# Kernel optimization log

Hardware: AMD Instinct MI355X
Metric: run time of the kernel (lower is better)

Reference implementation:

```python
import jax, jax.numpy as jnp
import numpy as np

NUM_HEADS = 32
NUM_KV = 8
Q_MULT = NUM_HEADS // NUM_KV  # 4
HEAD_DIM = 128
WINDOW = 1024
SM_SCALE = 1.0 / np.sqrt(HEAD_DIM)


def setup_inputs() -> dict:
    key = jax.random.key(0)
    k1, k2, k3, k4 = jax.random.split(key, 4)
    B, S = 2, 2048
    Q = jax.random.normal(k1, (B, S, NUM_HEADS * HEAD_DIM), dtype=jnp.float32)
    K = jax.random.normal(k2, (B, S, NUM_KV * HEAD_DIM), dtype=jnp.float32)
    V = jax.random.normal(k3, (B, S, NUM_KV * HEAD_DIM), dtype=jnp.float32)
    sinks = jax.random.normal(k4, (NUM_HEADS,), dtype=jnp.float32) * 0.1
    return {"Q": Q, "K": K, "V": V, "sinks": sinks}


def reference(Q, K, V, sinks):
    B, S, _ = Q.shape
    # GQA layout: head = kv * q_mult + m (matches Q[b].view(S, kv, q_mult, d))
    Qh = Q.reshape(B, S, NUM_KV, Q_MULT, HEAD_DIM)
    Kh = K.reshape(B, S, NUM_KV, HEAD_DIM)
    Vh = V.reshape(B, S, NUM_KV, HEAD_DIM)

    # scores: [B, kv, q_mult, S_q, S_k]
    scores = jnp.einsum('bqhmd,bkhd->bhmqk', Qh, Kh) * SM_SCALE

    q_idx = jnp.arange(S)[:, None]
    k_idx = jnp.arange(S)[None, :]
    # causal AND within sliding window: q - WINDOW < k <= q
    allowed = (k_idx <= q_idx) & (k_idx > q_idx - WINDOW)
    scores = jnp.where(allowed[None, None, None, :, :], scores, -jnp.inf)

    # learned sink logit per head, appended as an extra softmax column
    sink = sinks.reshape(NUM_KV, Q_MULT)[None, :, :, None, None]
    sink = jnp.broadcast_to(sink, (B, NUM_KV, Q_MULT, S, 1))
    logits = jnp.concatenate([scores, sink], axis=-1)
    w = jax.nn.softmax(logits, axis=-1)[..., :-1]  # drop sink column

    out = jnp.einsum('bhmqk,bkhd->bqhmd', w, Vh)
    return out.reshape(B, S, NUM_HEADS * HEAD_DIM)
```

## Files before the change

kernel.cpp:

```cpp
#include <hip/hip_runtime.h>
#include <stdint.h>

#define S_LEN 2048
#define HD    128
#define NKV   8
#define NQM   4
#define WIN   1024
#define QB    32
#define KTILE 32
#define KVROW (NKV * HD)
#define QROW  (NQM * NKV * HD)

typedef __attribute__((ext_vector_type(8))) short bf16x8;
typedef __attribute__((ext_vector_type(4))) float f32x4;
typedef __attribute__((ext_vector_type(4))) int   i32x4;

__device__ __forceinline__ uint32_t f2bf(float f) {
  uint32_t x = __builtin_bit_cast(uint32_t, f);
  x += 0x7fffu + ((x >> 16) & 1u);
  return x >> 16;
}

__device__ __forceinline__ void load8bf(const uint16_t* p, uint32_t o[4]) {
  i32x4 v = *reinterpret_cast<const i32x4*>(p);
  o[0] = (uint32_t)v[0]; o[1] = (uint32_t)v[1]; o[2] = (uint32_t)v[2]; o[3] = (uint32_t)v[3];
}
__device__ __forceinline__ void load8bf(const float* p, uint32_t o[4]) {
  float4 a = *reinterpret_cast<const float4*>(p);
  float4 b = *reinterpret_cast<const float4*>(p + 4);
  o[0] = f2bf(a.x) | (f2bf(a.y) << 16);
  o[1] = f2bf(a.z) | (f2bf(a.w) << 16);
  o[2] = f2bf(b.x) | (f2bf(b.y) << 16);
  o[3] = f2bf(b.z) | (f2bf(b.w) << 16);
}

__global__ void cvt_kernel(const float* __restrict__ in, uint16_t* __restrict__ out, int n4) {
  int i = blockIdx.x * blockDim.x + threadIdx.x;
  int stride = gridDim.x * blockDim.x;
  for (int j = i; j < n4; j += stride) {
    float4 v = reinterpret_cast<const float4*>(in)[j];
    ushort4 o;
    o.x = (uint16_t)f2bf(v.x); o.y = (uint16_t)f2bf(v.y);
    o.z = (uint16_t)f2bf(v.z); o.w = (uint16_t)f2bf(v.w);
    reinterpret_cast<ushort4*>(out)[j] = o;
  }
}

#define VSWZ(d) (((((uint32_t)(d) >> 3) ^ (uint32_t)(d)) & 7u) << 3)

template <typename KVT>
__launch_bounds__(256, 2)
__global__ void attn_kernel(const float* __restrict__ Q,
                            const KVT* __restrict__ Ksrc,
                            const KVT* __restrict__ Vsrc,
                            const float* __restrict__ sinks,
                            float* __restrict__ out) {
  __shared__ __align__(16) uint8_t smem[40960];

  const int tid  = threadIdx.x;
  const int lane = tid & 63;
  const int wv   = tid >> 6;
  const int c    = lane & 15;
  const int g    = lane >> 4;
  uint8_t* pls = smem + 32768 + wv * 2048;

  const int bid = blockIdx.x;
  const int kv  = bid & 7;
  const int i2  = bid >> 3;
  const int b   = i2 / 48;
  const int pairIdx = i2 % 48;
  const int head = kv * NQM + wv;
  const float sink_l2 = sinks[head] * 1.4426950408889634f;

  int qtA, qtB, nrep;
  if (pairIdx < 16) { qtA = 31 - pairIdx; qtB = pairIdx; nrep = 2; }
  else              { qtA = pairIdx + 16; qtB = 0;       nrep = 1; }

  const int kr  = tid >> 3;
  const int kcB = (tid & 7) * 32;
  const uint32_t kw0 = (uint32_t)(kr * 256 + ((kcB)      ^ ((kr & 7) << 4)));
  const uint32_t kw1 = (uint32_t)(kr * 256 + ((kcB + 16) ^ ((kr & 7) << 4)));
  const KVT* kg = Ksrc + (size_t)(b * S_LEN) * KVROW + kv * HD + (tid & 7) * 16;
  const size_t kbase = (size_t)(b * S_LEN) * KVROW + kv * HD;
  const int va = tid >> 4;
  const int vd = tid & 15;
  const KVT* vg = Vsrc + (size_t)(b * S_LEN) * KVROW + kv * HD + vd * 8;

  uint32_t vr0[4], vr1[4];

  auto stageK = [&](uint8_t* kbuf, int kt) {
    if constexpr (sizeof(KVT) == 2) {
      #pragma unroll
      for (int ch = 0; ch < 2; ++ch) {
        const int o    = wv * 2048 + ch * 1024 + lane * 16;
        const int row  = o >> 8;
        const int scol = (o & 255) ^ ((row & 7) << 4);
        const uint8_t* gp = (const uint8_t*)(Ksrc + kbase + (size_t)(kt + row) * KVROW) + scol;
        __builtin_amdgcn_global_load_lds(
            (const __attribute__((address_space(1))) void*)gp,
            (__attribute__((address_space(3))) void*)(kbuf + wv * 2048 + ch * 1024),
            16, 0, 0);
      }
    } else {
      const KVT* src = kg + (size_t)(kt + kr) * KVROW;
      uint32_t t0[4], t1[4];
      load8bf(src, t0); load8bf(src + 8, t1);
      i32x4 w0, w1;
      w0[0]=(int)t0[0]; w0[1]=(int)t0[1]; w0[2]=(int)t0[2]; w0[3]=(int)t0[3];
      w1[0]=(int)t1[0]; w1[1]=(int)t1[1]; w1[2]=(int)t1[2]; w1[3]=(int)t1[3];
      *reinterpret_cast<i32x4*>(kbuf + kw0) = w0;
      *reinterpret_cast<i32x4*>(kbuf + kw1) = w1;
    }
  };
  auto loadV = [&](int kt) {
    const KVT* vs = vg + (size_t)(kt + 2 * va) * KVROW;
    load8bf(vs, vr0); load8bf(vs + KVROW, vr1);
  };
  auto writeV = [&](uint8_t* vbuf) {
    #pragma unroll
    for (int ii = 0; ii < 8; ++ii) {
      int d = vd * 8 + ii;
      uint32_t lo = (ii & 1) ? (vr0[ii >> 1] >> 16) : (vr0[ii >> 1] & 0xffffu);
      uint32_t hi = (ii & 1) ? (vr1[ii >> 1] >> 16) : (vr1[ii >> 1] & 0xffffu);
      uint32_t byte = (uint32_t)(d * 64) + (((uint32_t)(va * 4)) ^ VSWZ(d));
      *reinterpret_cast<uint32_t*>(vbuf + byte) = lo | (hi << 16);
    }
  };

  const float SCALE2 = 0.08838834764831845f * 1.4426950408889634f;
  const uint32_t sp = ((uint32_t)(c & 7)) << 3;

  for (int rep = 0; rep < nrep; ++rep) {
    const int q0 = (rep ? qtB : qtA) * QB;

    bf16x8 qf[2][4];
    #pragma unroll
    for (int tq = 0; tq < 2; ++tq) {
      const float* qp = Q + (size_t)(b * S_LEN + q0 + tq * 16 + c) * QROW + head * HD;
      #pragma unroll
      for (int f = 0; f < 4; ++f) {
        int d0 = f * 32 + g * 8;
        float4 a = *reinterpret_cast<const float4*>(qp + d0);
        float4 bb = *reinterpret_cast<const float4*>(qp + d0 + 4);
        i32x4 t;
        t[0] = (int)(f2bf(a.x * SCALE2) | (f2bf(a.y * SCALE2) << 16));
        t[1] = (int)(f2bf(a.z * SCALE2) | (f2bf(a.w * SCALE2) << 16));
        t[2] = (int)(f2bf(bb.x * SCALE2) | (f2bf(bb.y * SCALE2) << 16));
        t[3] = (int)(f2bf(bb.z * SCALE2) | (f2bf(bb.w * SCALE2) << 16));
        qf[tq][f] = __builtin_bit_cast(bf16x8, t);
      }
    }

    float m_[2] = {sink_l2, sink_l2};
    float l_[2] = {1.0f, 1.0f};
    f32x4 acc[2][8];
    #pragma unroll
    for (int tq = 0; tq < 2; ++tq)
      #pragma unroll
      for (int dt = 0; dt < 8; ++dt) acc[tq][dt] = (f32x4)0.0f;

    int kstart = q0 - (WIN - 1);
    if (kstart < 0) kstart = 0;
    kstart &= ~(KTILE - 1);

    uint8_t* kcur = smem;         uint8_t* kalt = smem + 8192;
    uint8_t* vcur = smem + 16384; uint8_t* valt = smem + 24576;

    loadV(kstart);
    stageK(kcur, kstart);
    writeV(vcur);
    __syncthreads();

    for (int kt = kstart; kt <= q0; kt += KTILE) {
      const bool more = (kt + KTILE) <= q0;
      if (more) {
        stageK(kalt, kt + KTILE);
        loadV(kt + KTILE);
      }

      f32x4 st[2][2];
      #pragma unroll
      for (int a_ = 0; a_ < 2; ++a_)
        #pragma unroll
        for (int b_ = 0; b_ < 2; ++b_) st[a_][b_] = (f32x4)0.0f;

      __builtin_amdgcn_s_setprio(1);
      #pragma unroll
      for (int kt_ = 0; kt_ < 2; ++kt_) {
        bf16x8 kf[4];
        #pragma unroll
        for (int f = 0; f < 4; ++f) {
          int row = kt_ * 16 + c;
          uint32_t byte = (uint32_t)(row * 256 + ((f * 64 + g * 16) ^ ((row & 7) << 4)));
          kf[f] = *reinterpret_cast<const bf16x8*>(kcur + byte);
        }
        #pragma unroll
        for (int tq = 0; tq < 2; ++tq)
          #pragma unroll
          for (int f = 0; f < 4; ++f)
            st[kt_][tq] = __builtin_amdgcn_mfma_f32_16x16x32_bf16(kf[f], qf[tq][f], st[kt_][tq], 0, 0, 0);
      }
      __builtin_amdgcn_s_setprio(0);

      const bool need_mask = (kt + KTILE - 1 > q0) || (kt < q0 + QB - WIN);
      if (need_mask) {
        #pragma unroll
        for (int kt_ = 0; kt_ < 2; ++kt_)
          #pragma unroll
          for (int tq = 0; tq < 2; ++tq)
            #pragma unroll
            for (int r = 0; r < 4; ++r) {
              int k_ = kt + kt_ * 16 + g * 4 + r;
              int q_ = q0 + tq * 16 + c;
              bool ok = (k_ <= q_) && (k_ > q_ - WIN);
              if (!ok) st[kt_][tq][r] = -1e38f;
            }
      }

      #pragma unroll
      for (int tq = 0; tq < 2; ++tq) {
        float vmax = fmaxf(fmaxf(fmaxf(st[0][tq][0], st[0][tq][1]), fmaxf(st[0][tq][2], st[0][tq][3])),
                           fmaxf(fmaxf(st[1][tq][0], st[1][tq][1]), fmaxf(st[1][tq][2], st[1][tq][3])));
        vmax = fmaxf(vmax, __shfl_xor(vmax, 16));
        vmax = fmaxf(vmax, __shfl_xor(vmax, 32));
        const float mold = m_[tq];
        if (!__all(vmax <= mold + 11.54f)) {
          float mnew = fmaxf(mold, vmax);
          float scl  = exp2f(mold - mnew);
          m_[tq] = mnew;
          l_[tq] *= scl;
          float sc[4];
          #pragma unroll
          for (int r = 0; r < 4; ++r) sc[r] = __shfl(scl, (lane & 48) | (g * 4 + r));
          #pragma unroll
          for (int dt = 0; dt < 8; ++dt)
            #pragma unroll
            for (int r = 0; r < 4; ++r) acc[tq][dt][r] *= sc[r];
        }
        const float mrun = m_[tq];
        float p[2][4];
        float s = 0.0f;
        #pragma unroll
        for (int kt_ = 0; kt_ < 2; ++kt_)
          #pragma unroll
          for (int r = 0; r < 4; ++r) {
            float e = exp2f(st[kt_][tq][r] - mrun);
            p[kt_][r] = e;
            s += e;
          }
        s += __shfl_xor(s, 16);
        s += __shfl_xor(s, 32);
        l_[tq] += s;
        #pragma unroll
        for (int kt_ = 0; kt_ < 2; ++kt_) {
          uint32_t lo = f2bf(p[kt_][0]) | (f2bf(p[kt_][1]) << 16);
          uint32_t hi = f2bf(p[kt_][2]) | (f2bf(p[kt_][3]) << 16);
          uint32_t byte = (uint32_t)((tq * 16 + c) * 64) + (((uint32_t)(kt_ * 32 + g * 8)) ^ sp);
          uint2 pk; pk.x = lo; pk.y = hi;
          *reinterpret_cast<uint2*>(pls + byte) = pk;
        }
      }

      bf16x8 pa[2];
      #pragma unroll
      for (int tq = 0; tq < 2; ++tq) {
        uint32_t base = (uint32_t)((tq * 16 + c) * 64);
        uint2 plo = *reinterpret_cast<const uint2*>(pls + base + (((uint32_t)(g * 16))     ^ sp));
        uint2 phi = *reinterpret_cast<const uint2*>(pls + base + (((uint32_t)(g * 16 + 8)) ^ sp));
        i32x4 pv; pv[0] = (int)plo.x; pv[1] = (int)plo.y; pv[2] = (int)phi.x; pv[3] = (int)phi.y;
        pa[tq] = __builtin_bit_cast(bf16x8, pv);
      }
      __builtin_amdgcn_s_setprio(1);
      #pragma unroll
      for (int dt = 0; dt < 8; ++dt) {
        int d = dt * 16 + c;
        uint32_t rowb = (uint32_t)(d * 64);
        uint32_t swz  = VSWZ(d);
        uint2 lo = *reinterpret_cast<const uint2*>(vcur + rowb + (((uint32_t)(g * 16))     ^ swz));
        uint2 hi = *reinterpret_cast<const uint2*>(vcur + rowb + (((uint32_t)(g * 16 + 8)) ^ swz));
        i32x4 vv; vv[0] = (int)lo.x; vv[1] = (int)lo.y; vv[2] = (int)hi.x; vv[3] = (int)hi.y;
        bf16x8 vf = __builtin_bit_cast(bf16x8, vv);
        #pragma unroll
        for (int tq = 0; tq < 2; ++tq)
          acc[tq][dt] = __builtin_amdgcn_mfma_f32_16x16x32_bf16(pa[tq], vf, acc[tq][dt], 0, 0, 0);
      }
      __builtin_amdgcn_s_setprio(0);

      if (more) writeV(valt);
      __syncthreads();
      uint8_t* t0 = kcur; kcur = kalt; kalt = t0;
      uint8_t* t1 = vcur; vcur = valt; valt = t1;
    }

    #pragma unroll
    for (int tq = 0; tq < 2; ++tq) {
      float linv = 1.0f / l_[tq];
      float li[4];
      #pragma unroll
      for (int r = 0; r < 4; ++r) li[r] = __shfl(linv, (lane & 48) | (g * 4 + r));
      #pragma unroll
      for (int dt = 0; dt < 8; ++dt)
        #pragma unroll
        for (int r = 0; r < 4; ++r) {
          size_t o = (size_t)(b * S_LEN + q0 + tq * 16 + g * 4 + r) * QROW + head * HD + dt * 16 + c;
          out[o] = acc[tq][dt][r] * li[r];
        }
    }
  }
}

extern "C" void kernel_launch(void* const* d_in, const int* in_sizes, int n_in,
                              void* d_out, int out_size, void* d_ws, size_t ws_size,
                              hipStream_t stream) {
  const float* Q     = (const float*)d_in[0];
  const float* K     = (const float*)d_in[1];
  const float* V     = (const float*)d_in[2];
  const float* sinks = (const float*)d_in[3];
  float* out = (float*)d_out;

  const int nK = in_sizes[1];
  const int B  = in_sizes[0] / (S_LEN * QROW);
  dim3 grid(384 * B);

  const size_t need = (size_t)nK * 2u * 2u;
  if (ws_size >= need) {
    uint16_t* Kb = (uint16_t*)d_ws;
    uint16_t* Vb = Kb + nK;
    cvt_kernel<<<1024, 256, 0, stream>>>(K, Kb, nK / 4);
    cvt_kernel<<<1024, 256, 0, stream>>>(V, Vb, nK / 4);
    attn_kernel<uint16_t><<<grid, 256, 0, stream>>>(Q, Kb, Vb, sinks, out);
  } else {
    attn_kernel<float><<<grid, 256, 0, stream>>>(Q, K, V, sinks, out);
  }
}
```

Before: 247.3 us.

## Use packed bf16 convert, lane-local row sums, lazy max reduction, fused K/V conversion

Replaces the manual round-to-nearest bf16 packing with the hardware v_cvt_pk_bf16_f32 instruction, and uses v_perm_b32 to interleave V halves. The per-tile row-sum shuffles are removed: each lane keeps a partial sum (initialised to a quarter of the sink term) and the sum is reduced across lanes once at the end. The row-max cross-lane shuffles now run only when the lane-local max exceeds the threshold. The two K/V conversion launches are merged into one kernel. All of these are meant to cut VALU and shuffle work in the inner loop plus one launch, with a slight rounding-mode dependence on the hardware convert.

After: 226.4 us. -8.4%, faster.

```diff
diff --git a/kernel.cpp b/kernel.cpp
--- a/kernel.cpp
+++ b/kernel.cpp
@@ -21,6 +21,17 @@
   return x >> 16;
 }
 
+__device__ __forceinline__ uint32_t cvtpk(float lo, float hi) {
+  uint32_t r;
+  asm("v_cvt_pk_bf16_f32 %0, %1, %2" : "=v"(r) : "v"(lo), "v"(hi));
+  return r;
+}
+__device__ __forceinline__ uint32_t perm2(uint32_t a, uint32_t b, uint32_t sel) {
+  uint32_t r;
+  asm("v_perm_b32 %0, %1, %2, %3" : "=v"(r) : "v"(a), "v"(b), "s"(sel));
+  return r;
+}
+
 __device__ __forceinline__ void load8bf(const uint16_t* p, uint32_t o[4]) {
   i32x4 v = *reinterpret_cast<const i32x4*>(p);
   o[0] = (uint32_t)v[0]; o[1] = (uint32_t)v[1]; o[2] = (uint32_t)v[2]; o[3] = (uint32_t)v[3];
@@ -28,21 +39,25 @@
 __device__ __forceinline__ void load8bf(const float* p, uint32_t o[4]) {
   float4 a = *reinterpret_cast<const float4*>(p);
   float4 b = *reinterpret_cast<const float4*>(p + 4);
-  o[0] = f2bf(a.x) | (f2bf(a.y) << 16);
-  o[1] = f2bf(a.z) | (f2bf(a.w) << 16);
-  o[2] = f2bf(b.x) | (f2bf(b.y) << 16);
-  o[3] = f2bf(b.z) | (f2bf(b.w) << 16);
-}
-
-__global__ void cvt_kernel(const float* __restrict__ in, uint16_t* __restrict__ out, int n4) {
+  o[0] = cvtpk(a.x, a.y);
+  o[1] = cvtpk(a.z, a.w);
+  o[2] = cvtpk(b.x, b.y);
+  o[3] = cvtpk(b.z, b.w);
+}
+
+__global__ void cvt2_kernel(const float* __restrict__ inK, const float* __restrict__ inV,
+                            uint16_t* __restrict__ outK, uint16_t* __restrict__ outV, int n4) {
   int i = blockIdx.x * blockDim.x + threadIdx.x;
   int stride = gridDim.x * blockDim.x;
-  for (int j = i; j < n4; j += stride) {
-    float4 v = reinterpret_cast<const float4*>(in)[j];
-    ushort4 o;
-    o.x = (uint16_t)f2bf(v.x); o.y = (uint16_t)f2bf(v.y);
-    o.z = (uint16_t)f2bf(v.z); o.w = (uint16_t)f2bf(v.w);
-    reinterpret_cast<ushort4*>(out)[j] = o;
+  for (int j = i; j < 2 * n4; j += stride) {
+    const float* in = (j < n4) ? inK : inV;
+    uint16_t* out   = (j < n4) ? outK : outV;
+    int jj = (j < n4) ? j : j - n4;
+    float4 v = reinterpret_cast<const float4*>(in)[jj];
+    uint2 o;
+    o.x = cvtpk(v.x, v.y);
+    o.y = cvtpk(v.z, v.w);
+    reinterpret_cast<uint2*>(out)[jj] = o;
   }
 }
 
@@ -120,10 +135,10 @@
     #pragma unroll
     for (int ii = 0; ii < 8; ++ii) {
       int d = vd * 8 + ii;
-      uint32_t lo = (ii & 1) ? (vr0[ii >> 1] >> 16) : (vr0[ii >> 1] & 0xffffu);
-      uint32_t hi = (ii & 1) ? (vr1[ii >> 1] >> 16) : (vr1[ii >> 1] & 0xffffu);
+      uint32_t w = (ii & 1) ? perm2(vr1[ii >> 1], vr0[ii >> 1], 0x07060302u)
+                            : perm2(vr1[ii >> 1], vr0[ii >> 1], 0x05040100u);
       uint32_t byte = (uint32_t)(d * 64) + (((uint32_t)(va * 4)) ^ VSWZ(d));
-      *reinterpret_cast<uint32_t*>(vbuf + byte) = lo | (hi << 16);
+      *reinterpret_cast<uint32_t*>(vbuf + byte) = w;
     }
   };
 
@@ -143,16 +158,16 @@
         float4 a = *reinterpret_cast<const float4*>(qp + d0);
         float4 bb = *reinterpret_cast<const float4*>(qp + d0 + 4);
         i32x4 t;
-        t[0] = (int)(f2bf(a.x * SCALE2) | (f2bf(a.y * SCALE2) << 16));
-        t[1] = (int)(f2bf(a.z * SCALE2) | (f2bf(a.w * SCALE2) << 16));
-        t[2] = (int)(f2bf(bb.x * SCALE2) | (f2bf(bb.y * SCALE2) << 16));
-        t[3] = (int)(f2bf(bb.z * SCALE2) | (f2bf(bb.w * SCALE2) << 16));
+        t[0] = (int)cvtpk(a.x * SCALE2, a.y * SCALE2);
+        t[1] = (int)cvtpk(a.z * SCALE2, a.w * SCALE2);
+        t[2] = (int)cvtpk(bb.x * SCALE2, bb.y * SCALE2);
+        t[3] = (int)cvtpk(bb.z * SCALE2, bb.w * SCALE2);
         qf[tq][f] = __builtin_bit_cast(bf16x8, t);
       }
     }
 
     float m_[2] = {sink_l2, sink_l2};
-    float l_[2] = {1.0f, 1.0f};
+    float lp_[2] = {0.25f, 0.25f};
     f32x4 acc[2][8];
     #pragma unroll
     for (int tq = 0; tq < 2; ++tq)
@@ -219,16 +234,16 @@
 
       #pragma unroll
       for (int tq = 0; tq < 2; ++tq) {
-        float vmax = fmaxf(fmaxf(fmaxf(st[0][tq][0], st[0][tq][1]), fmaxf(st[0][tq][2], st[0][tq][3])),
-                           fmaxf(fmaxf(st[1][tq][0], st[1][tq][1]), fmaxf(st[1][tq][2], st[1][tq][3])));
-        vmax = fmaxf(vmax, __shfl_xor(vmax, 16));
-        vmax = fmaxf(vmax, __shfl_xor(vmax, 32));
+        float ownmax = fmaxf(fmaxf(fmaxf(st[0][tq][0], st[0][tq][1]), fmaxf(st[0][tq][2], st[0][tq][3])),
+                             fmaxf(fmaxf(st[1][tq][0], st[1][tq][1]), fmaxf(st[1][tq][2], st[1][tq][3])));
         const float mold = m_[tq];
-        if (!__all(vmax <= mold + 11.54f)) {
+        if (!__all(ownmax <= mold + 11.54f)) {
+          float vmax = fmaxf(ownmax, __shfl_xor(ownmax, 16));
+          vmax = fmaxf(vmax, __shfl_xor(vmax, 32));
           float mnew = fmaxf(mold, vmax);
           float scl  = exp2f(mold - mnew);
           m_[tq] = mnew;
-          l_[tq] *= scl;
+          lp_[tq] *= scl;
           float sc[4];
           #pragma unroll
           for (int r = 0; r < 4; ++r) sc[r] = __shfl(scl, (lane & 48) | (g * 4 + r));
@@ -248,15 +263,13 @@
             p[kt_][r] = e;
             s += e;
           }
-        s += __shfl_xor(s, 16);
-        s += __shfl_xor(s, 32);
-        l_[tq] += s;
+        lp_[tq] += s;
         #pragma unroll
         for (int kt_ = 0; kt_ < 2; ++kt_) {
-          uint32_t lo = f2bf(p[kt_][0]) | (f2bf(p[kt_][1]) << 16);
-          uint32_t hi = f2bf(p[kt_][2]) | (f2bf(p[kt_][3]) << 16);
+          uint2 pk;
+          pk.x = cvtpk(p[kt_][0], p[kt_][1]);
+          pk.y = cvtpk(p[kt_][2], p[kt_][3]);
           uint32_t byte = (uint32_t)((tq * 16 + c) * 64) + (((uint32_t)(kt_ * 32 + g * 8)) ^ sp);
-          uint2 pk; pk.x = lo; pk.y = hi;
           *reinterpret_cast<uint2*>(pls + byte) = pk;
         }
       }
@@ -294,7 +307,10 @@
 
     #pragma unroll
     for (int tq = 0; tq < 2; ++tq) {
-      float linv = 1.0f / l_[tq];
+      float lt = lp_[tq];
+      lt += __shfl_xor(lt, 16);
+      lt += __shfl_xor(lt, 32);
+      float linv = 1.0f / lt;
       float li[4];
       #pragma unroll
       for (int r = 0; r < 4; ++r) li[r] = __shfl(linv, (lane & 48) | (g * 4 + r));
@@ -326,8 +342,7 @@
   if (ws_size >= need) {
     uint16_t* Kb = (uint16_t*)d_ws;
     uint16_t* Vb = Kb + nK;
-    cvt_kernel<<<1024, 256, 0, stream>>>(K, Kb, nK / 4);
-    cvt_kernel<<<1024, 256, 0, stream>>>(V, Vb, nK / 4);
+    cvt2_kernel<<<1024, 256, 0, stream>>>(K, V, Kb, Vb, nK / 4);
     attn_kernel<uint16_t><<<grid, 256, 0, stream>>>(Q, Kb, Vb, sinks, out);
   } else {
     attn_kernel<float><<<grid, 256, 0, stream>>>(Q, K, V, sinks, out);
```
